# Performance work log

Measured on AMD Instinct MI355X. Metric: run time of the kernel, lower is better.

Reference implementation:

```python
import jax, jax.numpy as jnp
import numpy as np

NBIT = 4          # weight bit-width
GROUP_SIZE = 128  # weight quantization group size (divides k)
HAS_WEIGHT_ZEROS = True


def _quant_dequant_weights(w, group_size=GROUP_SIZE, nbit=NBIT, has_zeros=HAS_WEIGHT_ZEROS):
    # Mirrors torchao _quantize + quantize_per_channel_group, then dequantizes
    # (the native kernel dequantizes inline with the matmul; math is identical).
    qmin = -(1 << (nbit - 1))
    qmax = (1 << (nbit - 1)) - 1
    n, k = w.shape
    g = w.reshape(-1, group_size)                      # [n*k/gs, gs]
    vmin = g.min(axis=1, keepdims=True)
    vmax = g.max(axis=1, keepdims=True)
    scales = (vmax - vmin) / (qmax - qmin)             # per-group scale
    if has_zeros:
        zeros = qmin - jnp.round(vmin / scales)
    else:
        zeros = jnp.zeros_like(scales)
    q = jnp.clip(jnp.round(g / scales) + zeros, qmin, qmax)
    deq = (q - zeros) * scales
    return deq.reshape(n, k)


def _dyn_quant_dequant_act(x):
    # Dynamic per-token (per-row) asymmetric int8 activation quantization.
    qmin, qmax = -128, 127
    xmin = x.min(axis=-1, keepdims=True)
    xmax = x.max(axis=-1, keepdims=True)
    scale = (xmax - xmin) / (qmax - qmin)
    zero = qmin - jnp.round(xmin / scale)
    q = jnp.clip(jnp.round(x / scale) + zero, qmin, qmax)
    return (q - zero) * scale


def setup_inputs() -> dict:
    key = jax.random.key(0)
    k1, k2 = jax.random.split(key)
    x = jax.random.normal(k1, (4, 2048, 4096), dtype=jnp.float32)
    weights = jax.random.normal(k2, (4096, 4096), dtype=jnp.float32) * 0.02
    return {"x": x, "weights": weights}


def reference(x, weights):
    w_deq = _quant_dequant_weights(weights)            # [n, k]
    x_deq = _dyn_quant_dequant_act(x)                  # [..., m, k]
    # y[..., m, n] = x_deq @ w_deq^T
    return jnp.einsum('bmk,nk->bmn', x_deq, w_deq)
```

## Files before the change

kernel.cpp:

```cpp
#include <hip/hip_runtime.h>
#include <hip/hip_bf16.h>
#include <cfloat>

typedef __attribute__((ext_vector_type(8))) short bf16x8;
typedef __attribute__((ext_vector_type(4))) float f32x4;

#define M_DIM 8192
#define N_DIM 4096
#define K_DIM 4096

__device__ inline ushort f2bf(float f) {
    unsigned u = __float_as_uint(f);
    unsigned r = (u + 0x7FFFu + ((u >> 16) & 1u)) >> 16;
    return (ushort)r;
}

#define SWZ(x) ((x) ^ ((((x) >> 7) & 7) << 4))

__global__ __launch_bounds__(256) void w_dequant(const float* __restrict__ w,
                                                 ushort* __restrict__ wq) {
    int g = blockIdx.x * 4 + (threadIdx.x >> 6);
    int lane = threadIdx.x & 63;
    const float* src = w + (size_t)g * 128;
    float2 v = *(const float2*)(src + lane * 2);
    float mn = fminf(v.x, v.y), mx = fmaxf(v.x, v.y);
#pragma unroll
    for (int s = 1; s < 64; s <<= 1) {
        mn = fminf(mn, __shfl_xor(mn, s));
        mx = fmaxf(mx, __shfl_xor(mx, s));
    }
    float scale = (mx - mn) / 15.0f;
    float zero  = -8.0f - rintf(mn / scale);
    float q0 = fminf(fmaxf(rintf(v.x / scale) + zero, -8.0f), 7.0f);
    float q1 = fminf(fmaxf(rintf(v.y / scale) + zero, -8.0f), 7.0f);
    ushort2 o;
    o.x = f2bf((q0 - zero) * scale);
    o.y = f2bf((q1 - zero) * scale);
    *(ushort2*)(wq + (size_t)g * 128 + lane * 2) = o;
}

__global__ __launch_bounds__(256) void act_qdq(const float* __restrict__ x,
                                               ushort* __restrict__ xq) {
    __shared__ float smn[4], smx[4];
    int row = blockIdx.x;
    const float* xr = x + (size_t)row * K_DIM;
    ushort* xo = xq + (size_t)row * K_DIM;
    int t = threadIdx.x;
    float4 v[4];
    float mn = FLT_MAX, mx = -FLT_MAX;
#pragma unroll
    for (int i = 0; i < 4; i++) {
        v[i] = ((const float4*)xr)[t + i * 256];
        mn = fminf(mn, fminf(fminf(v[i].x, v[i].y), fminf(v[i].z, v[i].w)));
        mx = fmaxf(mx, fmaxf(fmaxf(v[i].x, v[i].y), fmaxf(v[i].z, v[i].w)));
    }
#pragma unroll
    for (int s = 1; s < 64; s <<= 1) {
        mn = fminf(mn, __shfl_xor(mn, s));
        mx = fmaxf(mx, __shfl_xor(mx, s));
    }
    int w = t >> 6;
    if ((t & 63) == 0) { smn[w] = mn; smx[w] = mx; }
    __syncthreads();
    mn = fminf(fminf(smn[0], smn[1]), fminf(smn[2], smn[3]));
    mx = fmaxf(fmaxf(smx[0], smx[1]), fmaxf(smx[2], smx[3]));
    float scale = (mx - mn) / 255.0f;
    float zero  = -128.0f - rintf(mn / scale);
#pragma unroll
    for (int i = 0; i < 4; i++) {
        ushort4 o;
        float q;
        q = fminf(fmaxf(rintf(v[i].x / scale) + zero, -128.0f), 127.0f); o.x = f2bf((q - zero) * scale);
        q = fminf(fmaxf(rintf(v[i].y / scale) + zero, -128.0f), 127.0f); o.y = f2bf((q - zero) * scale);
        q = fminf(fmaxf(rintf(v[i].z / scale) + zero, -128.0f), 127.0f); o.z = f2bf((q - zero) * scale);
        q = fminf(fmaxf(rintf(v[i].w / scale) + zero, -128.0f), 127.0f); o.w = f2bf((q - zero) * scale);
        ((ushort4*)xo)[t + i * 256] = o;
    }
}

#define BM 256
#define BN 256
#define BK 64
#define NT (K_DIM / BK)

__global__ __launch_bounds__(512, 1) void gemm_bt8(const ushort* __restrict__ A,
                                                   const ushort* __restrict__ B,
                                                   float* __restrict__ C) {
    __shared__ __align__(16) ushort As[2][BM * BK];
    __shared__ __align__(16) ushort Bs[2][BN * BK];

    const int nbx = N_DIM / BN;
    const int nwg = (M_DIM / BM) * nbx;
    int bid = blockIdx.x;
    bid = (bid & 7) * (nwg / 8) + (bid >> 3);
    int mb = bid / nbx, nb = bid % nbx;
    size_t m0 = (size_t)mb * BM, n0 = (size_t)nb * BN;

    const int t = threadIdx.x;
    const int w = t >> 6, lane = t & 63;
    const int wm = w >> 2, wn = w & 3;
    const int lr = lane & 15;
    const int lk = (lane >> 4) << 3;

    const ushort* Ab = A + m0 * K_DIM;
    const ushort* Bb = B + n0 * K_DIM;

    const int mask7 = (lr & 7) << 4;
    const int lp0 = lr * 128 + ((lk * 2) ^ mask7);
    const int lp1 = lr * 128 + ((64 + lk * 2) ^ mask7);
    const char* A_k0 = (const char*)As + wm * 4096 + lp0;
    const char* A_k1 = (const char*)As + wm * 4096 + lp1;
    const char* B_k0 = (const char*)Bs + wn * 8192 + lp0;
    const char* B_k1 = (const char*)Bs + wn * 8192 + lp1;

    int off_q[4], dst_q[4];
#pragma unroll
    for (int rq = 0; rq < 4; rq++) {
        int base = rq * 8192 + w * 1024;
        int lg = SWZ(base + lane * 16);
        off_q[rq] = (lg >> 7) * K_DIM + ((lg & 127) >> 1);
        dst_q[rq] = base;
    }

    auto STAGE = [&](int T, int qq) {
        if (T >= NT) return;
        int d = T & 1;
        bool isA = qq < 4;
        int rq = qq & 3;
        ushort* l = isA ? As[d] : Bs[d];
        const ushort* g = (isA ? Ab : Bb) + (size_t)T * BK + off_q[rq];
        __builtin_amdgcn_global_load_lds(
            (const __attribute__((address_space(1))) unsigned int*)g,
            (__attribute__((address_space(3))) unsigned int*)((char*)l + dst_q[rq]),
            16, 0, 0);
    };

    f32x4 acc[8][4] = {};
    bf16x8 afr[2][2][2];
    bf16x8 bfr[4][2];

#define LOADA(S, d, q) do {                                                       \
    _Pragma("unroll") for (int ii = 0; ii < 2; ii++)                              \
        afr[S][ii][0] = *(const bf16x8*)(A_k0 + (d) * 32768 + ((q) * 64 + ii * 16) * 128); \
    _Pragma("unroll") for (int ii = 0; ii < 2; ii++)                              \
        afr[S][ii][1] = *(const bf16x8*)(A_k1 + (d) * 32768 + ((q) * 64 + ii * 16) * 128); \
    } while (0)
#define LOADB(d) do {                                                             \
    _Pragma("unroll") for (int ni = 0; ni < 4; ni++)                              \
        bfr[ni][0] = *(const bf16x8*)(B_k0 + (d) * 32768 + ni * 2048);            \
    _Pragma("unroll") for (int ni = 0; ni < 4; ni++)                              \
        bfr[ni][1] = *(const bf16x8*)(B_k1 + (d) * 32768 + ni * 2048);            \
    } while (0)

#define PHASE(d, q, S, dn, qn, sT1, sq1, sT2, sq2, vm) do {                       \
    if ((q) == 0) LOADB(d);                                                       \
    LOADA((S) ^ 1, dn, qn);                                                       \
    STAGE(sT1, sq1);                                                              \
    STAGE(sT2, sq2);                                                              \
    __builtin_amdgcn_s_setprio(1);                                                \
    _Pragma("unroll") for (int kk = 0; kk < 2; kk++)                              \
    _Pragma("unroll") for (int ii = 0; ii < 2; ii++)                              \
    _Pragma("unroll") for (int ni = 0; ni < 4; ni++)                              \
        acc[(q) * 2 + ii][ni] = __builtin_amdgcn_mfma_f32_16x16x32_bf16(          \
            afr[S][ii][kk], bfr[ni][kk], acc[(q) * 2 + ii][ni], 0, 0, 0);         \
    __builtin_amdgcn_s_setprio(0);                                                \
    if ((vm) == 1) asm volatile("s_waitcnt vmcnt(6)" ::: "memory");               \
    if ((vm) == 2) asm volatile("s_waitcnt vmcnt(0)" ::: "memory");               \
    __builtin_amdgcn_s_barrier();                                                 \
  } while (0)

    STAGE(0, 0); STAGE(0, 1); STAGE(0, 2); STAGE(0, 3);
    STAGE(0, 4); STAGE(0, 5); STAGE(0, 6); STAGE(0, 7);
    STAGE(1, 4); STAGE(1, 5); STAGE(1, 6); STAGE(1, 7);
    STAGE(1, 0); STAGE(1, 1);
    asm volatile("s_waitcnt vmcnt(6)" ::: "memory");
    __builtin_amdgcn_s_barrier();
    LOADA(0, 0, 0);

#pragma unroll 1
    for (int i = 0; i < NT / 2 - 1; i++) {
        int T0 = 2 * i;
        PHASE(0, 0, 0, 0, 1, T0 + 1, 2, T0 + 1, 3, 1);
        PHASE(0, 1, 1, 0, 2, T0 + 2, 4, T0 + 2, 5, 1);
        PHASE(0, 2, 0, 0, 3, T0 + 2, 6, T0 + 2, 7, 1);
        PHASE(0, 3, 1, 1, 0, T0 + 2, 0, T0 + 2, 1, 1);
        PHASE(1, 0, 0, 1, 1, T0 + 2, 2, T0 + 2, 3, 1);
        PHASE(1, 1, 1, 1, 2, T0 + 3, 4, T0 + 3, 5, 1);
        PHASE(1, 2, 0, 1, 3, T0 + 3, 6, T0 + 3, 7, 1);
        PHASE(1, 3, 1, 0, 0, T0 + 3, 0, T0 + 3, 1, 1);
    }

    PHASE(0, 0, 0, 0, 1, NT - 1, 2, NT - 1, 3, 1);
    PHASE(0, 1, 1, 0, 2, NT, 0, NT, 0, 2);
    PHASE(0, 2, 0, 0, 3, NT, 0, NT, 0, 0);
    PHASE(0, 3, 1, 1, 0, NT, 0, NT, 0, 0);
    PHASE(1, 0, 0, 1, 1, NT, 0, NT, 0, 0);
    PHASE(1, 1, 1, 1, 2, NT, 0, NT, 0, 0);
    PHASE(1, 2, 0, 1, 3, NT, 0, NT, 0, 0);
    PHASE(1, 3, 1, 0, 0, NT, 0, NT, 0, 0);
#undef PHASE
#undef LOADA
#undef LOADB

    int fq = lane >> 4;
#pragma unroll
    for (int mi = 0; mi < 8; mi++) {
#pragma unroll
        for (int ni = 0; ni < 4; ni++) {
#pragma unroll
            for (int r = 0; r < 4; r++) {
                size_t crow = m0 + (mi >> 1) * 64 + wm * 32 + (mi & 1) * 16 + fq * 4 + r;
                C[crow * N_DIM + n0 + wn * 64 + ni * 16 + lr] = acc[mi][ni][r];
            }
        }
    }
}

extern "C" void kernel_launch(void* const* d_in, const int* in_sizes, int n_in,
                              void* d_out, int out_size, void* d_ws, size_t ws_size,
                              hipStream_t stream) {
    const float* x = (const float*)d_in[0];
    const float* w = (const float*)d_in[1];
    float* out = (float*)d_out;

    ushort* wq = (ushort*)d_ws;
    ushort* xq = (ushort*)((char*)d_ws + (size_t)N_DIM * K_DIM * 2);

    hipLaunchKernelGGL(w_dequant, dim3((N_DIM * K_DIM / 128) / 4), dim3(256), 0, stream, w, wq);
    hipLaunchKernelGGL(act_qdq, dim3(M_DIM), dim3(256), 0, stream, x, xq);
    hipLaunchKernelGGL(gemm_bt8, dim3((M_DIM / BM) * (N_DIM / BN)), dim3(512), 0, stream, xq, wq, out);
}
```

Before: 308.0 us.

## Restructure GEMM main loop to split K-halves per phase and drop A-fragment double buffering

Reorganizes the inner pipeline so each phase loads the A fragments for one K-half and one M-half directly before its MFMAs, instead of prefetching the next phase's A fragments into a double buffer. Global-to-LDS staging is regrouped so four stage loads are issued in one phase out of every two, and the vmcnt waits and prologue are adjusted to match. The M-row mapping of the accumulators is changed and the epilogue is updated for it. This cuts the fragment register footprint and simplifies the schedule, but it removes the overlap between LDS reads and MFMA work, so more of the LDS latency may be exposed.

Result: no change. 308.8 us (+0.3%).

```diff
diff --git a/kernel.cpp b/kernel.cpp
--- a/kernel.cpp
+++ b/kernel.cpp
@@ -108,10 +108,10 @@
     const int mask7 = (lr & 7) << 4;
     const int lp0 = lr * 128 + ((lk * 2) ^ mask7);
     const int lp1 = lr * 128 + ((64 + lk * 2) ^ mask7);
-    const char* A_k0 = (const char*)As + wm * 4096 + lp0;
-    const char* A_k1 = (const char*)As + wm * 4096 + lp1;
-    const char* B_k0 = (const char*)Bs + wn * 8192 + lp0;
-    const char* B_k1 = (const char*)Bs + wn * 8192 + lp1;
+    const char* A_kb[2] = { (const char*)As + wm * 4096 + lp0,
+                            (const char*)As + wm * 4096 + lp1 };
+    const char* B_kb[2] = { (const char*)Bs + wn * 8192 + lp0,
+                            (const char*)Bs + wn * 8192 + lp1 };
 
     int off_q[4], dst_q[4];
 #pragma unroll
@@ -136,35 +136,30 @@
     };
 
     f32x4 acc[8][4] = {};
-    bf16x8 afr[2][2][2];
-    bf16x8 bfr[4][2];
-
-#define LOADA(S, d, q) do {                                                       \
-    _Pragma("unroll") for (int ii = 0; ii < 2; ii++)                              \
-        afr[S][ii][0] = *(const bf16x8*)(A_k0 + (d) * 32768 + ((q) * 64 + ii * 16) * 128); \
-    _Pragma("unroll") for (int ii = 0; ii < 2; ii++)                              \
-        afr[S][ii][1] = *(const bf16x8*)(A_k1 + (d) * 32768 + ((q) * 64 + ii * 16) * 128); \
+    bf16x8 afr[4];
+    bf16x8 bfr[4];
+
+#define LOADA(d, kk, h) do {                                                      \
+    _Pragma("unroll") for (int j = 0; j < 4; j++)                                 \
+        afr[j] = *(const bf16x8*)(A_kb[kk] + (d) * 32768 + (h) * 16384            \
+                                  + (j >> 1) * 8192 + (j & 1) * 2048);            \
     } while (0)
-#define LOADB(d) do {                                                             \
+#define LOADB(d, kk) do {                                                         \
     _Pragma("unroll") for (int ni = 0; ni < 4; ni++)                              \
-        bfr[ni][0] = *(const bf16x8*)(B_k0 + (d) * 32768 + ni * 2048);            \
+        bfr[ni] = *(const bf16x8*)(B_kb[kk] + (d) * 32768 + ni * 2048);           \
+    } while (0)
+
+#define PHASE(d, kk, h, sT, qA, qB, qC, qD, vm) do {                              \
+    if ((h) == 0) LOADB(d, kk);                                                   \
+    LOADA(d, kk, h);                                                              \
+    STAGE(sT, qA); STAGE(sT, qB); STAGE(sT, qC); STAGE(sT, qD);                   \
+    __builtin_amdgcn_s_setprio(1);                                                \
+    _Pragma("unroll") for (int j = 0; j < 4; j++)                                 \
     _Pragma("unroll") for (int ni = 0; ni < 4; ni++)                              \
-        bfr[ni][1] = *(const bf16x8*)(B_k1 + (d) * 32768 + ni * 2048);            \
-    } while (0)
-
-#define PHASE(d, q, S, dn, qn, sT1, sq1, sT2, sq2, vm) do {                       \
-    if ((q) == 0) LOADB(d);                                                       \
-    LOADA((S) ^ 1, dn, qn);                                                       \
-    STAGE(sT1, sq1);                                                              \
-    STAGE(sT2, sq2);                                                              \
-    __builtin_amdgcn_s_setprio(1);                                                \
-    _Pragma("unroll") for (int kk = 0; kk < 2; kk++)                              \
-    _Pragma("unroll") for (int ii = 0; ii < 2; ii++)                              \
-    _Pragma("unroll") for (int ni = 0; ni < 4; ni++)                              \
-        acc[(q) * 2 + ii][ni] = __builtin_amdgcn_mfma_f32_16x16x32_bf16(          \
-            afr[S][ii][kk], bfr[ni][kk], acc[(q) * 2 + ii][ni], 0, 0, 0);         \
+        acc[(h) * 4 + j][ni] = __builtin_amdgcn_mfma_f32_16x16x32_bf16(           \
+            afr[j], bfr[ni], acc[(h) * 4 + j][ni], 0, 0, 0);                      \
     __builtin_amdgcn_s_setprio(0);                                                \
-    if ((vm) == 1) asm volatile("s_waitcnt vmcnt(6)" ::: "memory");               \
+    if ((vm) == 1) asm volatile("s_waitcnt vmcnt(4)" ::: "memory");               \
     if ((vm) == 2) asm volatile("s_waitcnt vmcnt(0)" ::: "memory");               \
     __builtin_amdgcn_s_barrier();                                                 \
   } while (0)
@@ -172,45 +167,46 @@
     STAGE(0, 0); STAGE(0, 1); STAGE(0, 2); STAGE(0, 3);
     STAGE(0, 4); STAGE(0, 5); STAGE(0, 6); STAGE(0, 7);
     STAGE(1, 4); STAGE(1, 5); STAGE(1, 6); STAGE(1, 7);
-    STAGE(1, 0); STAGE(1, 1);
-    asm volatile("s_waitcnt vmcnt(6)" ::: "memory");
+    asm volatile("s_waitcnt vmcnt(4)" ::: "memory");
     __builtin_amdgcn_s_barrier();
-    LOADA(0, 0, 0);
 
 #pragma unroll 1
     for (int i = 0; i < NT / 2 - 1; i++) {
-        int T0 = 2 * i;
-        PHASE(0, 0, 0, 0, 1, T0 + 1, 2, T0 + 1, 3, 1);
-        PHASE(0, 1, 1, 0, 2, T0 + 2, 4, T0 + 2, 5, 1);
-        PHASE(0, 2, 0, 0, 3, T0 + 2, 6, T0 + 2, 7, 1);
-        PHASE(0, 3, 1, 1, 0, T0 + 2, 0, T0 + 2, 1, 1);
-        PHASE(1, 0, 0, 1, 1, T0 + 2, 2, T0 + 2, 3, 1);
-        PHASE(1, 1, 1, 1, 2, T0 + 3, 4, T0 + 3, 5, 1);
-        PHASE(1, 2, 0, 1, 3, T0 + 3, 6, T0 + 3, 7, 1);
-        PHASE(1, 3, 1, 0, 0, T0 + 3, 0, T0 + 3, 1, 1);
-    }
-
-    PHASE(0, 0, 0, 0, 1, NT - 1, 2, NT - 1, 3, 1);
-    PHASE(0, 1, 1, 0, 2, NT, 0, NT, 0, 2);
-    PHASE(0, 2, 0, 0, 3, NT, 0, NT, 0, 0);
-    PHASE(0, 3, 1, 1, 0, NT, 0, NT, 0, 0);
-    PHASE(1, 0, 0, 1, 1, NT, 0, NT, 0, 0);
-    PHASE(1, 1, 1, 1, 2, NT, 0, NT, 0, 0);
-    PHASE(1, 2, 0, 1, 3, NT, 0, NT, 0, 0);
-    PHASE(1, 3, 1, 0, 0, NT, 0, NT, 0, 0);
+        int E = 2 * i;
+        PHASE(0, 0, 0, E + 1, 0, 1, 2, 3, 0);
+        PHASE(0, 0, 1, NT, 0, 0, 0, 0, 0);
+        PHASE(0, 1, 0, NT, 0, 0, 0, 0, 0);
+        PHASE(0, 1, 1, E + 2, 4, 5, 6, 7, 1);
+        PHASE(1, 0, 0, E + 2, 0, 1, 2, 3, 0);
+        PHASE(1, 0, 1, NT, 0, 0, 0, 0, 0);
+        PHASE(1, 1, 0, NT, 0, 0, 0, 0, 0);
+        PHASE(1, 1, 1, E + 3, 4, 5, 6, 7, 1);
+    }
+
+    PHASE(0, 0, 0, NT - 1, 0, 1, 2, 3, 0);
+    PHASE(0, 0, 1, NT, 0, 0, 0, 0, 0);
+    PHASE(0, 1, 0, NT, 0, 0, 0, 0, 0);
+    PHASE(0, 1, 1, NT, 0, 0, 0, 0, 2);
+    PHASE(1, 0, 0, NT, 0, 0, 0, 0, 0);
+    PHASE(1, 0, 1, NT, 0, 0, 0, 0, 0);
+    PHASE(1, 1, 0, NT, 0, 0, 0, 0, 0);
+    PHASE(1, 1, 1, NT, 0, 0, 0, 0, 0);
 #undef PHASE
 #undef LOADA
 #undef LOADB
 
     int fq = lane >> 4;
 #pragma unroll
-    for (int mi = 0; mi < 8; mi++) {
-#pragma unroll
-        for (int ni = 0; ni < 4; ni++) {
-#pragma unroll
-            for (int r = 0; r < 4; r++) {
-                size_t crow = m0 + (mi >> 1) * 64 + wm * 32 + (mi & 1) * 16 + fq * 4 + r;
-                C[crow * N_DIM + n0 + wn * 64 + ni * 16 + lr] = acc[mi][ni][r];
+    for (int h = 0; h < 2; h++) {
+#pragma unroll
+        for (int j = 0; j < 4; j++) {
+#pragma unroll
+            for (int ni = 0; ni < 4; ni++) {
+#pragma unroll
+                for (int r = 0; r < 4; r++) {
+                    size_t crow = m0 + h * 128 + (j >> 1) * 64 + wm * 32 + (j & 1) * 16 + fq * 4 + r;
+                    C[crow * N_DIM + n0 + wn * 64 + ni * 16 + lr] = acc[h * 4 + j][ni][r];
+                }
             }
         }
     }
```
